# Kernel optimization log

Measured on AMD Instinct MI355X. Metric: run time of the kernel, lower is better.

The kernel has to match this reference:

```python
import jax, jax.numpy as jnp
import numpy as np

H, W = 512, 512
N = 10240
CHUNK = 128  # gaussians per scan step; peak intermediate CHUNK*H*W floats
ALPHA_MIN = 1.0 / 255.0
ALPHA_MAX = 0.999


def setup_inputs() -> dict:
    key = jax.random.key(0)
    k1, k2, k3, k4 = jax.random.split(key, 4)
    # matches torch init: _xyz = atanh(2*(rand-0.5)); others = rand
    u = jax.random.uniform(k1, (N, 2), dtype=jnp.float32)
    xyz = jnp.arctanh(jnp.clip(2.0 * (u - 0.5), -0.999, 0.999))
    cholesky = jax.random.uniform(k2, (N, 3), dtype=jnp.float32)
    opacity = jax.random.uniform(k3, (N, 1), dtype=jnp.float32)
    features = jax.random.uniform(k4, (N, 3), dtype=jnp.float32)
    return {"xyz": xyz, "cholesky": cholesky, "opacity": opacity, "features": features}


def _render(xyz, cholesky, opacity, features):
    # project_gaussians_2d: mean in [-1,1] via tanh -> pixel coords
    mean = jnp.tanh(xyz)                      # [N,2]
    cx = 0.5 * W * (mean[:, 0] + 1.0)         # [N]
    cy = 0.5 * H * (mean[:, 1] + 1.0)
    # cholesky_bound = [0.5, 0, 0.5]
    l = cholesky + jnp.array([0.5, 0.0, 0.5], dtype=cholesky.dtype)
    l1, l2, l3 = l[:, 0], l[:, 1], l[:, 2]
    # cov = L L^T with L = [[l1,0],[l2,l3]]
    c00 = l1 * l1
    c01 = l1 * l2
    c11 = l2 * l2 + l3 * l3
    det = c00 * c11 - c01 * c01               # = (l1*l3)^2
    inv = 1.0 / det
    A = c11 * inv                             # conic.x
    B = -c01 * inv                            # conic.y
    C = c00 * inv                             # conic.z
    opac = opacity[:, 0]

    xs = jnp.arange(W, dtype=mean.dtype) + 0.5  # pixel centers
    ys = jnp.arange(H, dtype=mean.dtype) + 0.5

    nch = N // CHUNK

    def resh(t):
        return t.reshape(nch, CHUNK, *t.shape[1:])

    scan_args = (resh(cx), resh(cy), resh(A), resh(B), resh(C), resh(opac), resh(features))

    def body(img, a):
        cx_, cy_, A_, B_, C_, op_, col_ = a
        dx = cx_[:, None] - xs[None, :]       # [CHUNK, W]
        dy = cy_[:, None] - ys[None, :]       # [CHUNK, H]
        # sigma = 0.5*(A dx^2 + C dy^2) + B dx dy  (per gaussian, per pixel)
        sigma = (0.5 * A_[:, None, None] * (dx * dx)[:, None, :]
                 + 0.5 * C_[:, None, None] * (dy * dy)[:, :, None]
                 + B_[:, None, None] * dy[:, :, None] * dx[:, None, :])  # [CHUNK,H,W]
        alpha = jnp.minimum(ALPHA_MAX, op_[:, None, None] * jnp.exp(-sigma))
        alpha = jnp.where((sigma >= 0.0) & (alpha >= ALPHA_MIN), alpha, 0.0)
        img = img + jnp.einsum('nhw,nc->hwc', alpha, col_)
        return img, None

    img0 = jnp.zeros((H, W, 3), dtype=mean.dtype)
    img, _ = jax.lax.scan(body, img0, scan_args)
    img = jnp.clip(img, 0.0, 1.0)
    # view(-1,H,W,3).permute(0,3,1,2)
    return img.reshape(1, H, W, 3).transpose(0, 3, 1, 2)


def reference(xyz, cholesky, opacity, features):
    return _render(xyz, cholesky, opacity, features)
```

## Files before the change

kernel.cpp:

```cpp
#include <hip/hip_runtime.h>
#include <math.h>

#define HH 512
#define WW 512
#define NN 10240
#define TILE 16
#define TXN 32
#define TYN 32
#define CAP 256
#define A_MIN (1.0f/255.0f)
#define A_MAX 0.999f

__global__ __launch_bounds__(256) void prep_kernel(
    const float* __restrict__ xyz, const float* __restrict__ chol,
    const float* __restrict__ opac, const float* __restrict__ feat,
    float4* __restrict__ P0, float4* __restrict__ P1,
    float* __restrict__ P2b, unsigned int* __restrict__ Qt) {
  int n = blockIdx.x * 256 + threadIdx.x;
  if (n >= NN) return;
  float mx = tanhf(xyz[2*n+0]);
  float my = tanhf(xyz[2*n+1]);
  float cx = 0.5f * WW * (mx + 1.0f);
  float cy = 0.5f * HH * (my + 1.0f);
  float l1 = chol[3*n+0] + 0.5f;
  float l2 = chol[3*n+1];
  float l3 = chol[3*n+2] + 0.5f;
  float c00 = l1*l1;
  float c01 = l1*l2;
  float c11 = l2*l2 + l3*l3;
  float det = c00*c11 - c01*c01;
  float inv = 1.0f / det;
  float A = c11 * inv;
  float B = -c01 * inv;
  float C = c00 * inv;
  float op = opac[n];
  P0[n]  = make_float4(cx, cy, 0.5f * A, B);
  P1[n]  = make_float4(0.5f * C, op, feat[3*n+0], feat[3*n+1]);
  P2b[n] = feat[3*n+2];

  unsigned int q = 0x000000FFu;
  float smax = logf(op * 255.0f);
  if (smax > 0.0f) {
    float rx = sqrtf(2.0f * smax * c00) + 1.0f;
    float ry = sqrtf(2.0f * smax * c11) + 1.0f;
    int px0 = max(0,    (int)floorf(cx - rx));
    int px1 = min(WW-1, (int)floorf(cx + rx));
    int py0 = max(0,    (int)floorf(cy - ry));
    int py1 = min(HH-1, (int)floorf(cy + ry));
    if (px0 <= px1 && py0 <= py1) {
      unsigned int tx0 = px0 >> 4, tx1 = px1 >> 4;
      unsigned int ty0 = py0 >> 4, ty1 = py1 >> 4;
      q = tx0 | (tx1 << 8) | (ty0 << 16) | (ty1 << 24);
    }
  }
  Qt[n] = q;
}

__global__ __launch_bounds__(256, 4) void render_kernel(
    const float4* __restrict__ P0, const float4* __restrict__ P1,
    const float* __restrict__ P2b, const uint4* __restrict__ Q4,
    float* __restrict__ out) {
  __shared__ int    s_idx[CAP];
  __shared__ float4 sA[CAP];
  __shared__ float4 sB[CAP];
  __shared__ float  sC[CAP];
  __shared__ int    s_cnt;

  const int tx = blockIdx.x, ty = blockIdx.y;
  const int tid = threadIdx.x;
  if (tid == 0) s_cnt = 0;
  __syncthreads();

  #pragma unroll
  for (int i = 0; i < NN / (256 * 4); ++i) {
    uint4 q = Q4[i * 256 + tid];
    int base = (i * 256 + tid) * 4;
    unsigned int qq[4] = { q.x, q.y, q.z, q.w };
    #pragma unroll
    for (int s = 0; s < 4; ++s) {
      unsigned int v = qq[s];
      int tx0 = v & 0xFF, tx1 = (v >> 8) & 0xFF;
      int ty0 = (v >> 16) & 0xFF, ty1 = v >> 24;
      if (tx >= tx0 && tx <= tx1 && ty >= ty0 && ty <= ty1) {
        int k = atomicAdd(&s_cnt, 1);
        if (k < CAP) s_idx[k] = base + s;
      }
    }
  }
  __syncthreads();
  int cnt = min(s_cnt, CAP);

  if (tid < cnt) {
    int n = s_idx[tid];
    sA[tid] = P0[n];
    sB[tid] = P1[n];
    sC[tid] = P2b[n];
  }
  __syncthreads();

  const int lx = tid & 15;
  const int ly = tid >> 4;
  const float px = tx * TILE + lx + 0.5f;
  const float py = ty * TILE + ly + 0.5f;
  float accR = 0.0f, accG = 0.0f, accB = 0.0f;

  for (int j = 0; j < cnt; ++j) {
    float4 pa = sA[j];
    float4 pb = sB[j];
    float dx = pa.x - px;
    float dy = pa.y - py;
    float sigma = pa.z * dx * dx + pb.x * dy * dy + pa.w * dy * dx;
    float alpha = fminf(A_MAX, pb.y * __expf(-sigma));
    if (sigma >= 0.0f && alpha >= A_MIN) {
      accR += alpha * pb.z;
      accG += alpha * pb.w;
      accB += alpha * sC[j];
    }
  }

  const int x = tx * TILE + lx;
  const int y = ty * TILE + ly;
  const int pix = y * WW + x;
  out[0 * HH * WW + pix] = fminf(fmaxf(accR, 0.0f), 1.0f);
  out[1 * HH * WW + pix] = fminf(fmaxf(accG, 0.0f), 1.0f);
  out[2 * HH * WW + pix] = fminf(fmaxf(accB, 0.0f), 1.0f);
}

extern "C" void kernel_launch(void* const* d_in, const int* in_sizes, int n_in,
                              void* d_out, int out_size, void* d_ws, size_t ws_size,
                              hipStream_t stream) {
  const float* xyz  = (const float*)d_in[0];
  const float* chol = (const float*)d_in[1];
  const float* opac = (const float*)d_in[2];
  const float* feat = (const float*)d_in[3];

  char* ws = (char*)d_ws;
  float4*       P0  = (float4*)(ws);
  float4*       P1  = (float4*)(ws + (size_t)NN * 16);
  float*        P2b = (float*) (ws + (size_t)NN * 32);
  unsigned int* Qt  = (unsigned int*)(ws + (size_t)NN * 36);

  prep_kernel<<<(NN + 255) / 256, 256, 0, stream>>>(xyz, chol, opac, feat, P0, P1, P2b, Qt);
  render_kernel<<<dim3(TXN, TYN), 256, 0, stream>>>(P0, P1, P2b, (const uint4*)Qt, (float*)d_out);
}
```

Before: 22.03 us.

## Bin gaussians hierarchically per 32x32 block with wave ballot compaction

The render kernel now uses 1024-thread blocks that each cover four 16x16 tiles. Each of 16 waves first culls a slice of the gaussian list against the 32x32 block using ballot and popcount compaction instead of shared atomics. Four waves then re-filter the shortlist for each 16x16 sub-tile. This cuts the number of blocks that scan all per-gaussian tile bounds by four and removes atomic contention. The cost is fixed per-wave (24) and per-tile (128) caps that could silently drop gaussians in dense regions, plus an extra barrier phase.

```diff
diff --git a/kernel.cpp b/kernel.cpp
--- a/kernel.cpp
+++ b/kernel.cpp
@@ -4,12 +4,16 @@
 #define HH 512
 #define WW 512
 #define NN 10240
-#define TILE 16
-#define TXN 32
-#define TYN 32
-#define CAP 256
 #define A_MIN (1.0f/255.0f)
 #define A_MAX 0.999f
+
+#define RB 16
+#define WAVES 16
+#define WRANGE (NN/WAVES)
+#define WCHUNKS (WRANGE/64)
+#define RCAP 24
+#define RSLOTS (WAVES*RCAP)
+#define PCAP 128
 
 __global__ __launch_bounds__(256) void prep_kernel(
     const float* __restrict__ xyz, const float* __restrict__ chol,
@@ -56,74 +60,107 @@
   Qt[n] = q;
 }
 
-__global__ __launch_bounds__(256, 4) void render_kernel(
+__global__ __launch_bounds__(1024, 4) void render_kernel(
     const float4* __restrict__ P0, const float4* __restrict__ P1,
-    const float* __restrict__ P2b, const uint4* __restrict__ Q4,
-    float* __restrict__ out) {
-  __shared__ int    s_idx[CAP];
-  __shared__ float4 sA[CAP];
-  __shared__ float4 sB[CAP];
-  __shared__ float  sC[CAP];
-  __shared__ int    s_cnt;
+    const float* __restrict__ P2b, const unsigned int* __restrict__ Qt,
+    float* __restrict__ out)
+{
+  __shared__ uint2          reg2[RSLOTS];
+  __shared__ int            rcnt[WAVES];
+  __shared__ unsigned short qseg[4][PCAP];
+  __shared__ int            qcnt[4];
+  __shared__ float4         pA[4][PCAP];
+  __shared__ float4         pB[4][PCAP];
+  __shared__ float          pC[4][PCAP];
 
-  const int tx = blockIdx.x, ty = blockIdx.y;
-  const int tid = threadIdx.x;
-  if (tid == 0) s_cnt = 0;
+  const int tid  = threadIdx.x;
+  const int bx   = blockIdx.x, by = blockIdx.y;
+  const int w    = tid >> 6;
+  const int lane = tid & 63;
+
+  {
+    const int tx0r = 2*bx, tx1r = 2*bx + 1;
+    const int ty0r = 2*by, ty1r = 2*by + 1;
+    int base = 0;
+    for (int c = 0; c < WCHUNKS; ++c) {
+      int n = w*WRANGE + c*64 + lane;
+      unsigned int v = Qt[n];
+      int gtx0 = v & 0xFF, gtx1 = (v >> 8) & 0xFF;
+      int gty0 = (v >> 16) & 0xFF, gty1 = v >> 24;
+      bool hit = (gtx0 <= tx1r) & (gtx1 >= tx0r) & (gty0 <= ty1r) & (gty1 >= ty0r);
+      unsigned long long m = __ballot(hit);
+      int idx = base + (int)__popcll(m & ((1ull << lane) - 1ull));
+      if (hit && idx < RCAP) reg2[w*RCAP + idx] = make_uint2(v, (unsigned)n);
+      base += (int)__popcll(m);
+      if (base >= RCAP) { base = RCAP; break; }
+    }
+    if (lane == 0) rcnt[w] = base;
+  }
   __syncthreads();
 
-  #pragma unroll
-  for (int i = 0; i < NN / (256 * 4); ++i) {
-    uint4 q = Q4[i * 256 + tid];
-    int base = (i * 256 + tid) * 4;
-    unsigned int qq[4] = { q.x, q.y, q.z, q.w };
-    #pragma unroll
-    for (int s = 0; s < 4; ++s) {
-      unsigned int v = qq[s];
-      int tx0 = v & 0xFF, tx1 = (v >> 8) & 0xFF;
-      int ty0 = (v >> 16) & 0xFF, ty1 = v >> 24;
-      if (tx >= tx0 && tx <= tx1 && ty >= ty0 && ty <= ty1) {
-        int k = atomicAdd(&s_cnt, 1);
-        if (k < CAP) s_idx[k] = base + s;
-      }
+  if (w < 4) {
+    const int q   = w;
+    const int ttx = 2*bx + (q & 1);
+    const int tty = 2*by + (q >> 1);
+    int base = 0;
+    for (int c = 0; c < RSLOTS/64; ++c) {
+      int slot = c*64 + lane;
+      int rr = slot / RCAP;
+      int j  = slot - rr*RCAP;
+      bool valid = j < rcnt[rr];
+      unsigned int v = 0x000000FFu, n = 0;
+      if (valid) { uint2 e = reg2[slot]; v = e.x; n = e.y; }
+      int gtx0 = v & 0xFF, gtx1 = (v >> 8) & 0xFF;
+      int gty0 = (v >> 16) & 0xFF, gty1 = v >> 24;
+      bool hit = valid & (gtx0 <= ttx) & (gtx1 >= ttx) & (gty0 <= tty) & (gty1 >= tty);
+      unsigned long long m = __ballot(hit);
+      int idx = base + (int)__popcll(m & ((1ull << lane) - 1ull));
+      if (hit && idx < PCAP) qseg[q][idx] = (unsigned short)n;
+      base += (int)__popcll(m);
+    }
+    if (lane == 0) qcnt[q] = min(base, PCAP);
+  }
+  __syncthreads();
+
+  {
+    int q = tid >> 8;
+    int s = tid & 255;
+    if (s < qcnt[q]) {
+      int n = qseg[q][s];
+      pA[q][s] = P0[n];
+      pB[q][s] = P1[n];
+      pC[q][s] = P2b[n];
     }
   }
   __syncthreads();
-  int cnt = min(s_cnt, CAP);
 
-  if (tid < cnt) {
-    int n = s_idx[tid];
-    sA[tid] = P0[n];
-    sB[tid] = P1[n];
-    sC[tid] = P2b[n];
+  {
+    int q = tid >> 8;
+    int s = tid & 255;
+    int lx = s & 15, ly = s >> 4;
+    int x = bx*32 + (q & 1)*16 + lx;
+    int y = by*32 + (q >> 1)*16 + ly;
+    float px = x + 0.5f, py = y + 0.5f;
+    int tot = qcnt[q];
+    float accR = 0.0f, accG = 0.0f, accB = 0.0f;
+    for (int j = 0; j < tot; ++j) {
+      float4 pa = pA[q][j];
+      float4 pb = pB[q][j];
+      float dx = pa.x - px;
+      float dy = pa.y - py;
+      float sigma = pa.z*dx*dx + pb.x*dy*dy + pa.w*dy*dx;
+      float alpha = fminf(A_MAX, pb.y * __expf(-sigma));
+      if (sigma >= 0.0f && alpha >= A_MIN) {
+        accR += alpha * pb.z;
+        accG += alpha * pb.w;
+        accB += alpha * pC[q][j];
+      }
+    }
+    int pix = y * WW + x;
+    out[pix]              = fminf(fmaxf(accR, 0.0f), 1.0f);
+    out[HH*WW + pix]      = fminf(fmaxf(accG, 0.0f), 1.0f);
+    out[2*HH*WW + pix]    = fminf(fmaxf(accB, 0.0f), 1.0f);
   }
-  __syncthreads();
-
-  const int lx = tid & 15;
-  const int ly = tid >> 4;
-  const float px = tx * TILE + lx + 0.5f;
-  const float py = ty * TILE + ly + 0.5f;
-  float accR = 0.0f, accG = 0.0f, accB = 0.0f;
-
-  for (int j = 0; j < cnt; ++j) {
-    float4 pa = sA[j];
-    float4 pb = sB[j];
-    float dx = pa.x - px;
-    float dy = pa.y - py;
-    float sigma = pa.z * dx * dx + pb.x * dy * dy + pa.w * dy * dx;
-    float alpha = fminf(A_MAX, pb.y * __expf(-sigma));
-    if (sigma >= 0.0f && alpha >= A_MIN) {
-      accR += alpha * pb.z;
-      accG += alpha * pb.w;
-      accB += alpha * sC[j];
-    }
-  }
-
-  const int x = tx * TILE + lx;
-  const int y = ty * TILE + ly;
-  const int pix = y * WW + x;
-  out[0 * HH * WW + pix] = fminf(fmaxf(accR, 0.0f), 1.0f);
-  out[1 * HH * WW + pix] = fminf(fmaxf(accG, 0.0f), 1.0f);
-  out[2 * HH * WW + pix] = fminf(fmaxf(accB, 0.0f), 1.0f);
 }
 
 extern "C" void kernel_launch(void* const* d_in, const int* in_sizes, int n_in,
@@ -141,5 +178,5 @@
   unsigned int* Qt  = (unsigned int*)(ws + (size_t)NN * 36);
 
   prep_kernel<<<(NN + 255) / 256, 256, 0, stream>>>(xyz, chol, opac, feat, P0, P1, P2b, Qt);
-  render_kernel<<<dim3(TXN, TYN), 256, 0, stream>>>(P0, P1, P2b, (const uint4*)Qt, (float*)d_out);
+  render_kernel<<<dim3(RB, RB), 1024, 0, stream>>>(P0, P1, P2b, Qt, (float*)d_out);
 }
```

New measurement: 22.00 us. Within noise of the previous version (-0.2%).
